# Kernel tuning notes

Measured on AMD Instinct MI355X. Metric: run time of the kernel, lower is better.

Reference implementation:

```python
import jax, jax.numpy as jnp
import numpy as np

B, N, D, H = 2, 256, 512, 8
DK = D // H


def _lin(x, w, b):
    # torch nn.Linear: y = x @ W.T + b, W is [out, in]
    return jnp.matmul(x, w.T) + b


def setup_inputs() -> dict:
    key = jax.random.key(0)
    ks = jax.random.split(key, 12)
    std = 0.02
    inp = {
        "x": jax.random.normal(ks[0], (B, N, D), jnp.float32),
        "batched_graphs": jax.random.normal(ks[1], (B, N, N, D), jnp.float32) * std,
        "mask": jnp.zeros((B, N, N), dtype=bool),
    }
    names = ["wq", "wk", "wv", "wo", "wl", "wr", "wrk", "wrv"]
    for i, n in enumerate(names):
        inp[n] = jax.random.normal(ks[2 + i], (D, D), jnp.float32) * std
        inp["b" + n[1:]] = jnp.zeros((D,), jnp.float32)
    return inp


def reference(x, batched_graphs, mask,
              wq, bq, wk, bk, wv, bv, wo, bo,
              wl, bl, wr, br, wrk, brk, wrv, brv):
    # update_relations: per-edge key/value maps
    graphs_k = _lin(batched_graphs, wrk, brk).reshape(B, N, N, H, DK)
    graphs_v = _lin(batched_graphs, wrv, brv).reshape(B, N, N, H, DK)

    query = _lin(x, wq, bq).reshape(B, N, H, DK)
    key_ = _lin(x, wk, bk).reshape(B, N, H, DK)
    value = _lin(x, wv, bv).reshape(B, N, H, DK)

    scores_k = jnp.einsum("bxhd,byhd->bxyh", query, key_)
    scores_g = jnp.einsum("bxhd,bxyhd->bxyh", query, graphs_k)
    scores = (scores_k + scores_g) / np.sqrt(DK).astype(np.float32)
    scores = jnp.where(mask[..., None], jnp.float32(-1e9), scores)
    p_attn = jax.nn.softmax(scores, axis=2)  # over key nodes y

    x_v = jnp.einsum("bxyh,byhd->bxhd", p_attn, value)
    x_g = jnp.einsum("bxyh,bxyhd->bxhd", p_attn, graphs_v)
    out = (x_v + x_g).reshape(B, N, D)

    # relation update: outer sum of left/right projections
    x_left = _lin(out, wl, bl)[:, :, None, :]   # [B,N,1,D]
    x_right = _lin(out, wr, br)[:, None, :, :]  # [B,1,N,D]
    new_graphs = x_left + x_right               # [B,N,N,D]

    return _lin(out, wo, bo), new_graphs
```

## Files before the change

### kernel.cpp

```cpp
#include <hip/hip_runtime.h>

#define BB 2
#define NN 256
#define DD 512
#define HH 8

#define SCL 0.18033688f

typedef float f4raw __attribute__((ext_vector_type(4)));

__device__ __forceinline__ float dot4(float4 a, float4 b) {
    return a.x*b.x + a.y*b.y + a.z*b.z + a.w*b.w;
}

__device__ __forceinline__ float4 f4fma(float s, float4 a, float4 acc) {
    acc.x += s * a.x; acc.y += s * a.y; acc.z += s * a.z; acc.w += s * a.w;
    return acc;
}

__device__ __forceinline__ float4 f4mul(float s, float4 a) {
    a.x *= s; a.y *= s; a.z *= s; a.w *= s; return a;
}

__device__ __forceinline__ float4 f4add(float4 a, float4 b) {
    a.x += b.x; a.y += b.y; a.z += b.z; a.w += b.w; return a;
}

__device__ __forceinline__ void gload_lds16(const void* g, void* l) {
    __builtin_amdgcn_global_load_lds(
        (const __attribute__((address_space(1))) unsigned int*)g,
        (__attribute__((address_space(3))) unsigned int*)l, 16, 0, 0);
}

__device__ __forceinline__ void stage_swz(const char* rowbase, float4* dst, int w, int lane) {
    #pragma unroll
    for (int j = 0; j < 4; ++j) {
        const int f0 = w * 256 + j * 64;
        const int y = f0 >> 7;
        const int c = (f0 & 127) + lane;
        gload_lds16(rowbase + (size_t)y * 2048 + ((size_t)(c ^ y) << 4), &dst[f0]);
    }
}

__device__ __forceinline__ void stageG(const char* Grow, int tt, int w, int lane, float4* dst) {
    #pragma unroll
    for (int r = 0; r < 2; ++r) {
        const int yr = 2 * w + r;
        const char* src = Grow + (size_t)(tt * 8 + yr) * 2048;
        #pragma unroll
        for (int j = 0; j < 2; ++j) {
            const int c = j * 64 + lane;
            gload_lds16(src + ((size_t)(c ^ yr) << 4), &dst[r * 128 + j * 64]);
        }
    }
}

__global__ __launch_bounds__(64) void kProj(
    const float* __restrict__ in_,
    const float* __restrict__ w0, const float* __restrict__ b0,
    const float* __restrict__ w1, const float* __restrict__ b1,
    const float* __restrict__ w2, const float* __restrict__ b2,
    float* __restrict__ o0, float* __restrict__ o1, float* __restrict__ o2)
{
    __shared__ float4 xs[2][32 * 5];
    __shared__ float4 ws[2][32 * 5];

    const int t = threadIdx.x;
    const int blk = blockIdx.x;
    const int proj = blk >> 8;
    const int rem = blk & 255;
    const int row0 = (rem >> 4) * 32;
    const int col0 = (rem & 15) * 32;

    const float* W; const float* Bp; float* O;
    if (proj == 0)      { W = w0; Bp = b0; O = o0; }
    else if (proj == 1) { W = w1; Bp = b1; O = o1; }
    else                { W = w2; Bp = b2; O = o2; }

    const float4* X4 = (const float4*)in_ + (size_t)row0 * 128;
    const float4* W4 = (const float4*)W  + (size_t)col0 * 128;

    const int sr = t >> 2, se = t & 3;
    const int ty = t >> 3, tx = t & 7;

    float4 rx0 = X4[(size_t)sr * 128 + se];
    float4 rx1 = X4[(size_t)(sr + 16) * 128 + se];
    float4 rw0 = W4[(size_t)sr * 128 + se];
    float4 rw1 = W4[(size_t)(sr + 16) * 128 + se];
    xs[0][sr * 5 + se] = rx0;  xs[0][(sr + 16) * 5 + se] = rx1;
    ws[0][sr * 5 + se] = rw0;  ws[0][(sr + 16) * 5 + se] = rw1;

    float acc[4][4] = {};

    for (int q = 0; q < 32; ++q) {
        __syncthreads();
        const int cur = q & 1;
        if (q < 31) {
            const int ko = (q + 1) * 4;
            rx0 = X4[(size_t)sr * 128 + ko + se];
            rx1 = X4[(size_t)(sr + 16) * 128 + ko + se];
            rw0 = W4[(size_t)sr * 128 + ko + se];
            rw1 = W4[(size_t)(sr + 16) * 128 + ko + se];
        }
        const float4* xb = xs[cur];
        const float4* wb = ws[cur];
        #pragma unroll
        for (int e4 = 0; e4 < 4; ++e4) {
            float4 xr[4], wc[4];
            #pragma unroll
            for (int i = 0; i < 4; ++i) xr[i] = xb[(ty + 8 * i) * 5 + e4];
            #pragma unroll
            for (int j = 0; j < 4; ++j) wc[j] = wb[(tx + 8 * j) * 5 + e4];
            #pragma unroll
            for (int i = 0; i < 4; ++i)
                #pragma unroll
                for (int j = 0; j < 4; ++j)
                    acc[i][j] += dot4(xr[i], wc[j]);
        }
        if (q < 31) {
            const int nxt = cur ^ 1;
            xs[nxt][sr * 5 + se] = rx0;  xs[nxt][(sr + 16) * 5 + se] = rx1;
            ws[nxt][sr * 5 + se] = rw0;  ws[nxt][(sr + 16) * 5 + se] = rw1;
        }
    }

    float bb[4];
    #pragma unroll
    for (int j = 0; j < 4; ++j) bb[j] = Bp[col0 + tx + 8 * j];
    #pragma unroll
    for (int i = 0; i < 4; ++i) {
        const int orow = row0 + ty + 8 * i;
        #pragma unroll
        for (int j = 0; j < 4; ++j)
            O[(size_t)orow * DD + col0 + tx + 8 * j] = acc[i][j] + bb[j];
    }
}

__global__ __launch_bounds__(256) void kQkp(
    const float* __restrict__ q, const float* __restrict__ wrk,
    float* __restrict__ qkp)
{
    __shared__ float qs[8 * 64];
    const int t = threadIdx.x;
    const int blk = blockIdx.x;
    const int rowg = blk >> 5;
    const int h = (blk >> 2) & 7;
    const int eq = blk & 3;
    const int row0 = rowg * 8;
    {
        const int r = t >> 5, d2 = (t & 31) * 2;
        const float2 tmp = *(const float2*)(q + (size_t)(row0 + r) * DD + h * 64 + d2);
        qs[r * 64 + d2] = tmp.x; qs[r * 64 + d2 + 1] = tmp.y;
    }
    __syncthreads();
    const int e = eq * 128 + (t & 127);
    const int rp = (t >> 7) * 4;
    const float* wcol = wrk + (size_t)(h * 64) * DD + e;
    float a0 = 0, a1 = 0, a2 = 0, a3 = 0;
    #pragma unroll 8
    for (int d = 0; d < 64; ++d) {
        const float wv = wcol[(size_t)d * DD];
        a0 += qs[(rp + 0) * 64 + d] * wv;
        a1 += qs[(rp + 1) * 64 + d] * wv;
        a2 += qs[(rp + 2) * 64 + d] * wv;
        a3 += qs[(rp + 3) * 64 + d] * wv;
    }
    qkp[((size_t)(row0 + rp + 0) * HH + h) * DD + e] = a0;
    qkp[((size_t)(row0 + rp + 1) * HH + h) * DD + e] = a1;
    qkp[((size_t)(row0 + rp + 2) * HH + h) * DD + e] = a2;
    qkp[((size_t)(row0 + rp + 3) * HH + h) * DD + e] = a3;
}

__global__ __launch_bounds__(256) void kSk(
    const float* __restrict__ q, const float* __restrict__ k,
    const unsigned char* __restrict__ mask, float* __restrict__ sk)
{
    __shared__ float qs[8 * 65];
    __shared__ float ks[64 * 65];
    const int t = threadIdx.x;
    const int blk = blockIdx.x;
    const int b  = blk >> 10;
    const int h  = (blk >> 7) & 7;
    const int xt = (blk >> 2) & 31;
    const int yt = blk & 3;
    const int x0 = xt * 8, y0 = yt * 64;
    {
        const int r = t >> 5, d2 = (t & 31) * 2;
        const float2 tmp = *(const float2*)(q + (size_t)(b * NN + x0 + r) * DD + h * 64 + d2);
        qs[r * 65 + d2] = tmp.x; qs[r * 65 + d2 + 1] = tmp.y;
    }
    #pragma unroll
    for (int j = 0; j < 8; ++j) {
        const int f = t + 256 * j;
        const int r = f >> 5, d2 = (f & 31) * 2;
        const float2 tmp = *(const float2*)(k + (size_t)(b * NN + y0 + r) * DD + h * 64 + d2);
        ks[r * 65 + d2] = tmp.x; ks[r * 65 + d2 + 1] = tmp.y;
    }
    __syncthreads();
    const int xi = t >> 5, yg = t & 31;
    float a0 = 0, a1 = 0;
    #pragma unroll 8
    for (int d = 0; d < 64; ++d) {
        const float qv = qs[xi * 65 + d];
        a0 += qv * ks[(yg * 2 + 0) * 65 + d];
        a1 += qv * ks[(yg * 2 + 1) * 65 + d];
    }
    a0 *= SCL; a1 *= SCL;
    const unsigned char* mrow = mask + (size_t)(b * NN + x0 + xi) * NN;
    const int gy = y0 + yg * 2;
    if (mrow[gy + 0]) a0 = -1e9f;
    if (mrow[gy + 1]) a1 = -1e9f;
    float2 st; st.x = a0; st.y = a1;
    *(float2*)(sk + ((size_t)(b * NN + x0 + xi) * HH + h) * NN + gy) = st;
}

__global__ __launch_bounds__(256, 2) void kC(
    const float* __restrict__ G, const float* __restrict__ sk,
    const float* __restrict__ qkp, const float* __restrict__ v,
    float* __restrict__ pg, float* __restrict__ pxv,
    float* __restrict__ pm, float* __restrict__ pl)
{
    __shared__ float4 Gdb[2][4][256];
    __shared__ float4 qk4[1024];
    __shared__ float  sk_lds[512];
    __shared__ float  s_st[512];

    const int t = threadIdx.x;
    const int lane = t & 63;
    const int w = t >> 6;
    const int blk = blockIdx.x;
    const int part = blk & 3;
    const int bid = blk >> 2;
    const int b = bid >> 8;
    const int ybase = part * 64;

    const int s_ = lane & 15;
    const int g  = lane >> 4;
    const int h0_ = 2 * g, h1_ = h0_ + 1;
    const int yr0 = 2 * w, yr1 = yr0 + 1;

    const char* Grow = (const char*)(G + (size_t)bid * NN * DD) + (size_t)ybase * 2048;
    const float* skb = sk + (size_t)bid * HH * NN;
    const float4* vb4 = (const float4*)(v + (size_t)(b * NN) * DD);

    const int f0p = 2 * t, f1p = 2 * t + 1;
    const float skv0 = skb[(f0p & 7) * NN + ybase + (f0p >> 3)];
    const float skv1 = skb[(f1p & 7) * NN + ybase + (f1p >> 3)];
    stage_swz((const char*)(qkp + (size_t)bid * HH * DD), qk4, w, lane);
    float4 va0 = vb4[(size_t)(ybase + yr0) * 128 + 32 * g + s_];
    float4 vb0 = vb4[(size_t)(ybase + yr0) * 128 + 32 * g + 16 + s_];
    float4 va1 = vb4[(size_t)(ybase + yr1) * 128 + 32 * g + s_];
    float4 vb1 = vb4[(size_t)(ybase + yr1) * 128 + 32 * g + 16 + s_];
    stageG(Grow, 0, w, lane, &Gdb[0][w][0]);
    asm volatile("s_waitcnt vmcnt(4)" ::: "memory");
    __builtin_amdgcn_sched_barrier(0);
    sk_lds[f0p] = skv0;
    sk_lds[f1p] = skv1;
    __syncthreads();

    float4 gA[8], gB[8];
    float m[8], l[8];
    #pragma unroll
    for (int h = 0; h < 8; ++h) {
        gA[h] = make_float4(0, 0, 0, 0);
        gB[h] = make_float4(0, 0, 0, 0);
        m[h] = -3e38f; l[h] = 0.f;
    }
    float4 xva = {0, 0, 0, 0}, xvb = {0, 0, 0, 0};
    float4 nva0 = va0, nvb0 = vb0, nva1 = va1, nvb1 = vb1;

    int cb = 0;
    #pragma unroll 1
    for (int tt = 0; tt < 8; ++tt) {
        const int ry0 = tt * 8 + yr0, ry1 = ry0 + 1;

        __builtin_amdgcn_sched_barrier(0);
        if (tt < 7) {
            stageG(Grow, tt + 1, w, lane, &Gdb[cb ^ 1][w][0]);
            const int ngy0 = ybase + (tt + 1) * 8 + yr0;
            nva0 = vb4[(size_t)ngy0 * 128 + 32 * g + s_];
            nvb0 = vb4[(size_t)ngy0 * 128 + 32 * g + 16 + s_];
            nva1 = vb4[(size_t)(ngy0 + 1) * 128 + 32 * g + s_];
            nvb1 = vb4[(size_t)(ngy0 + 1) * 128 + 32 * g + 16 + s_];
            asm volatile("s_waitcnt vmcnt(8)" ::: "memory");
        } else {
            asm volatile("s_waitcnt vmcnt(0)" ::: "memory");
        }
        __builtin_amdgcn_sched_barrier(0);

        const float4* gb = &Gdb[cb][w][0];

        {
            float a00 = 0, a01 = 0, a10 = 0, a11 = 0;
            #pragma unroll
            for (int i = 0; i < 8; ++i) {
                const int e4 = i * 16 + s_;
                const float4 g0 = gb[(e4 ^ yr0)];
                const float4 g1 = gb[128 + (e4 ^ yr1)];
                const float4 p0 = qk4[h0_ * 128 + (e4 ^ h0_)];
                const float4 p1 = qk4[h1_ * 128 + (e4 ^ h1_)];
                a00 += dot4(g0, p0); a01 += dot4(g0, p1);
                a10 += dot4(g1, p0); a11 += dot4(g1, p1);
            }
            #pragma unroll
            for (int mm = 1; mm < 16; mm <<= 1) {
                a00 += __shfl_xor(a00, mm); a01 += __shfl_xor(a01, mm);
                a10 += __shfl_xor(a10, mm); a11 += __shfl_xor(a11, mm);
            }
            if (s_ < 4) {
                const int yy = s_ & 1, hh = s_ >> 1;
                const float val = yy ? (hh ? a11 : a10) : (hh ? a01 : a00);
                const int h = h0_ + hh;
                const int ry = yy ? ry1 : ry0;
                s_st[ry * 8 + h] = val * SCL + sk_lds[ry * 8 + h];
            }
        }

        const float4 sva = *(const float4*)&s_st[ry0 * 8];
        const float4 svb = *(const float4*)&s_st[ry0 * 8 + 4];
        const float4 svc = *(const float4*)&s_st[ry1 * 8];
        const float4 svd = *(const float4*)&s_st[ry1 * 8 + 4];
        const float s0[8] = {sva.x, sva.y, sva.z, sva.w, svb.x, svb.y, svb.z, svb.w};
        const float s1[8] = {svc.x, svc.y, svc.z, svc.w, svd.x, svd.y, svd.z, svd.w};

        const float4 gr0a = gb[(lane ^ yr0)];
        const float4 gr0b = gb[((lane + 64) ^ yr0)];
        const float4 gr1a = gb[128 + (lane ^ yr1)];
        const float4 gr1b = gb[128 + ((lane + 64) ^ yr1)];

        float p0a = 0, p1a = 0, rsa = 1, p0b = 0, p1b = 0, rsb = 1;
        #pragma unroll
        for (int h = 0; h < 8; ++h) {
            const float mn = fmaxf(m[h], fmaxf(s0[h], s1[h]));
            const float rs = exp2f(m[h] - mn);
            const float p0 = exp2f(s0[h] - mn);
            const float p1 = exp2f(s1[h] - mn);
            m[h] = mn;
            l[h] = l[h] * rs + p0 + p1;
            gA[h] = f4fma(p1, gr1a, f4fma(p0, gr0a, f4mul(rs, gA[h])));
            gB[h] = f4fma(p1, gr1b, f4fma(p0, gr0b, f4mul(rs, gB[h])));
            if (h == h0_) { p0a = p0; p1a = p1; rsa = rs; }
            if (h == h1_) { p0b = p0; p1b = p1; rsb = rs; }
        }
        xva = f4fma(p1a, va1, f4fma(p0a, va0, f4mul(rsa, xva)));
        xvb = f4fma(p1b, vb1, f4fma(p0b, vb0, f4mul(rsb, xvb)));
        va0 = nva0; vb0 = nvb0; va1 = nva1; vb1 = nvb1;
        cb ^= 1;
    }

    asm volatile("s_waitcnt vmcnt(0)" ::: "memory");
    __syncthreads();
    float* ml = sk_lds;
    if (lane == 0) {
        #pragma unroll
        for (int h = 0; h < 8; ++h) { ml[w * 16 + h] = m[h]; ml[w * 16 + 8 + h] = l[h]; }
    }
    __syncthreads();

    float ea = 1.f, eb = 1.f;
    float Mv[8], Lv[8];
    #pragma unroll
    for (int h = 0; h < 8; ++h) {
        const float q0 = ml[h], q1 = ml[16 + h], q2 = ml[32 + h], q3 = ml[48 + h];
        const float Mh = fmaxf(fmaxf(q0, q1), fmaxf(q2, q3));
        const float Lh = exp2f(q0 - Mh) * ml[8 + h]  + exp2f(q1 - Mh) * ml[24 + h]
                       + exp2f(q2 - Mh) * ml[40 + h] + exp2f(q3 - Mh) * ml[56 + h];
        Mv[h] = Mh; Lv[h] = Lh;
        const float e = exp2f(m[h] - Mh);
        gA[h] = f4mul(e, gA[h]);
        gB[h] = f4mul(e, gB[h]);
        if (h == h0_) ea = e;
        if (h == h1_) eb = e;
    }
    xva = f4mul(ea, xva);
    xvb = f4mul(eb, xvb);

    float4* rA = &Gdb[0][0][0];
    float4* rB = &Gdb[1][0][0];
    float4* xs_ = qk4;
    xs_[w * 128 + 32 * g + s_] = xva;
    xs_[w * 128 + 32 * g + 16 + s_] = xvb;
    if (w == 2) {
        #pragma unroll
        for (int h = 0; h < 8; ++h) { rA[h * 128 + lane] = gA[h]; rA[h * 128 + 64 + lane] = gB[h]; }
    }
    if (w == 3) {
        #pragma unroll
        for (int h = 0; h < 8; ++h) { rB[h * 128 + lane] = gA[h]; rB[h * 128 + 64 + lane] = gB[h]; }
    }
    __syncthreads();
    if (w == 0) {
        #pragma unroll
        for (int h = 0; h < 8; ++h) {
            gA[h] = f4add(gA[h], rA[h * 128 + lane]);
            gB[h] = f4add(gB[h], rA[h * 128 + 64 + lane]);
        }
    }
    if (w == 1) {
        #pragma unroll
        for (int h = 0; h < 8; ++h) {
            gA[h] = f4add(gA[h], rB[h * 128 + lane]);
            gB[h] = f4add(gB[h], rB[h * 128 + 64 + lane]);
        }
    }
    __syncthreads();
    if (w == 1) {
        #pragma unroll
        for (int h = 0; h < 8; ++h) { rA[h * 128 + lane] = gA[h]; rA[h * 128 + 64 + lane] = gB[h]; }
    }
    __syncthreads();
    if (w == 0) {
        float4* pgb = (float4*)pg + (size_t)blk * 1024;
        #pragma unroll
        for (int h = 0; h < 8; ++h) {
            gA[h] = f4add(gA[h], rA[h * 128 + lane]);
            gB[h] = f4add(gB[h], rA[h * 128 + 64 + lane]);
            pgb[h * 128 + lane] = gA[h];
            pgb[h * 128 + 64 + lane] = gB[h];
        }
        float4 xa = f4add(f4add(xs_[32 * g + s_],            xs_[128 + 32 * g + s_]),
                          f4add(xs_[256 + 32 * g + s_],      xs_[384 + 32 * g + s_]));
        float4 xb = f4add(f4add(xs_[32 * g + 16 + s_],       xs_[128 + 32 * g + 16 + s_]),
                          f4add(xs_[256 + 32 * g + 16 + s_], xs_[384 + 32 * g + 16 + s_]));
        float4* pxb = (float4*)pxv + (size_t)blk * 128;
        pxb[32 * g + s_] = xa;
        pxb[32 * g + 16 + s_] = xb;
        if (lane == 0) {
            #pragma unroll
            for (int h = 0; h < 8; ++h) { pm[blk * 8 + h] = Mv[h]; pl[blk * 8 + h] = Lv[h]; }
        }
    }
}

__global__ __launch_bounds__(256) void kM(
    const float* __restrict__ pg, const float* __restrict__ pxv,
    const float* __restrict__ pm, const float* __restrict__ pl,
    const float* __restrict__ wrv, const float* __restrict__ brv,
    float* __restrict__ om)
{
    __shared__ float4 gc[512];
    __shared__ float xvs[256];
    __shared__ float wexp[16], Ls[4];
    const int t = threadIdx.x;
    const int blk = blockIdx.x;
    const int bid = blk >> 1;
    const int half = blk & 1;
    const int h0 = half * 4;
    __shared__ float mlds[16], llds[16];
    if (t < 16) {
        const int i = t >> 2, hh = t & 3;
        mlds[t] = pm[bid * 32 + i * 8 + h0 + hh];
        llds[t] = pl[bid * 32 + i * 8 + h0 + hh];
    }
    __syncthreads();
    if (t < 4) {
        float M = mlds[t];
        #pragma unroll
        for (int i = 1; i < 4; ++i) M = fmaxf(M, mlds[i * 4 + t]);
        float L = 0;
        #pragma unroll
        for (int i = 0; i < 4; ++i) {
            const float wv = exp2f(mlds[i * 4 + t] - M);
            wexp[i * 4 + t] = wv;
            L += wv * llds[i * 4 + t];
        }
        Ls[t] = L;
    }
    __syncthreads();
    const int c4 = t & 127;
    #pragma unroll
    for (int r = 0; r < 2; ++r) {
        const int hh = (t >> 7) * 2 + r;
        float4 acc = {0, 0, 0, 0};
        #pragma unroll
        for (int i = 0; i < 4; ++i) {
            const float wv = wexp[i * 4 + hh];
            const float4 g = ((const float4*)pg)[((size_t)bid * 4 + i) * 1024 + (size_t)(h0 + hh) * 128 + c4];
            acc.x += wv * g.x; acc.y += wv * g.y; acc.z += wv * g.z; acc.w += wv * g.w;
        }
        gc[hh * 128 + c4] = acc;
    }
    {
        const int hh = t >> 6;
        float s = 0;
        #pragma unroll
        for (int i = 0; i < 4; ++i)
            s += wexp[i * 4 + hh] * pxv[((size_t)bid * 4 + i) * DD + half * 256 + t];
        xvs[t] = s;
    }
    __syncthreads();
    const int o = half * 256 + t;
    const int hl = t >> 6;
    const float4* wr4 = (const float4*)(wrv + (size_t)o * DD);
    float acc = 0;
    #pragma unroll 4
    for (int e4 = 0; e4 < 128; ++e4) acc += dot4(wr4[e4], gc[hl * 128 + e4]);
    om[(size_t)bid * DD + o] = (xvs[t] + acc) / Ls[hl] + brv[o];
}

__global__ __launch_bounds__(256) void kE(
    const float* __restrict__ xl, const float* __restrict__ xr,
    float* __restrict__ ng)
{
    const int t = threadIdx.x;
    const int blk = blockIdx.x;
    const int bid = blk >> 2;
    const int yc = blk & 3;
    const int b = bid >> 8;
    const int o4 = t & 127;
    const int yh = t >> 7;
    const float4 left = ((const float4*)xl)[(size_t)bid * 128 + o4];
    const float4* xr4 = (const float4*)xr + (size_t)b * NN * 128;
    f4raw* out4 = (f4raw*)ng + (size_t)bid * NN * 128;
    for (int y = yc * 64 + yh; y < yc * 64 + 64; y += 2) {
        const float4 rr = xr4[y * 128 + o4];
        f4raw s;
        s.x = left.x + rr.x; s.y = left.y + rr.y;
        s.z = left.z + rr.z; s.w = left.w + rr.w;
        __builtin_nontemporal_store(s, &out4[y * 128 + o4]);
    }
}

extern "C" void kernel_launch(void* const* d_in, const int* in_sizes, int n_in,
                              void* d_out, int out_size, void* d_ws, size_t ws_size,
                              hipStream_t stream)
{
    (void)in_sizes; (void)n_in; (void)out_size; (void)ws_size;
    const float* x    = (const float*)d_in[0];
    const float* G    = (const float*)d_in[1];
    const unsigned char* mask = (const unsigned char*)d_in[2];
    const float* wq  = (const float*)d_in[3];  const float* bq  = (const float*)d_in[4];
    const float* wk  = (const float*)d_in[5];  const float* bk  = (const float*)d_in[6];
    const float* wv  = (const float*)d_in[7];  const float* bv  = (const float*)d_in[8];
    const float* wo  = (const float*)d_in[9];  const float* bo  = (const float*)d_in[10];
    const float* wl  = (const float*)d_in[11]; const float* bl  = (const float*)d_in[12];
    const float* wr  = (const float*)d_in[13]; const float* br  = (const float*)d_in[14];
    const float* wrk = (const float*)d_in[15];
    const float* wrv = (const float*)d_in[17]; const float* brv = (const float*)d_in[18];

    float* out  = (float*)d_out;
    float* fout = out;
    float* ng   = out + (size_t)BB * NN * DD;

    const size_t ng_f  = (size_t)BB * NN * NN * DD;
    const size_t row_f = (size_t)BB * NN * DD;
    const size_t total = row_f * 52 + 32768;
    float* base = ng + ng_f - total;
    float* q    = base;
    float* k    = q   + row_f;
    float* vv_  = k   + row_f;
    float* qkp  = vv_ + row_f;
    float* skp  = qkp + row_f * 8;
    float* pg   = skp + row_f * 4;
    float* pxv  = pg  + row_f * 32;
    float* pm   = pxv + row_f * 4;
    float* pl   = pm  + 16384;
    float* om   = pl  + 16384;
    float* xl = (float*)d_ws;
    float* xr = xl + row_f;

    kProj<<<768, 64, 0, stream>>>(x, wq, bq, wk, bk, wv, bv, q, k, vv_);
    kQkp <<<2048, 256, 0, stream>>>(q, wrk, qkp);
    kSk  <<<2048, 256, 0, stream>>>(q, k, mask, skp);
    kC   <<<2048, 256, 0, stream>>>(G, skp, qkp, vv_, pg, pxv, pm, pl);
    kM   <<<1024, 256, 0, stream>>>(pg, pxv, pm, pl, wrv, brv, om);
    kProj<<<768, 64, 0, stream>>>(om, wo, bo, wl, bl, wr, br, fout, xl, xr);
    kE   <<<2048, 256, 0, stream>>>(xl, xr, ng);
}
```

Baseline: 311.1 us.

## Merge qkp and score kernels; process one graph row per wave per step in kC

Folds the kQkp and kSk launches into one kernel, kQS, that picks its role from the block index, removing one launch and letting both workloads run side by side. In kC, each wave now handles one G row per iteration over 16 steps instead of two rows over 8. This halves the G double buffer in LDS and cuts register pressure, since V is loaded inside the loop rather than prefetched. The cross-wave reduction becomes a serial loop over three stages. The trade-off is more loop iterations and barriers, and V loads that are no longer prefetched and may stall each step.

```diff
diff --git a/kernel.cpp b/kernel.cpp
--- a/kernel.cpp
+++ b/kernel.cpp
@@ -42,16 +42,12 @@
     }
 }
 
-__device__ __forceinline__ void stageG(const char* Grow, int tt, int w, int lane, float4* dst) {
-    #pragma unroll
-    for (int r = 0; r < 2; ++r) {
-        const int yr = 2 * w + r;
-        const char* src = Grow + (size_t)(tt * 8 + yr) * 2048;
-        #pragma unroll
-        for (int j = 0; j < 2; ++j) {
-            const int c = j * 64 + lane;
-            gload_lds16(src + ((size_t)(c ^ yr) << 4), &dst[r * 128 + j * 64]);
-        }
+__device__ __forceinline__ void stageG1(const char* Grow, int tt, int w, int lane, float4* dst) {
+    const char* src = Grow + (size_t)(tt * 4 + w) * 2048;
+    #pragma unroll
+    for (int j = 0; j < 2; ++j) {
+        const int c = j * 64 + lane;
+        gload_lds16(src + ((size_t)(c ^ w) << 4), &dst[j * 64]);
     }
 }
 
@@ -136,82 +132,81 @@
     }
 }
 
-__global__ __launch_bounds__(256) void kQkp(
+__global__ __launch_bounds__(256) void kQS(
     const float* __restrict__ q, const float* __restrict__ wrk,
-    float* __restrict__ qkp)
+    const float* __restrict__ k, const unsigned char* __restrict__ mask,
+    float* __restrict__ qkp, float* __restrict__ sk)
 {
-    __shared__ float qs[8 * 64];
+    __shared__ float sm[4680];
     const int t = threadIdx.x;
-    const int blk = blockIdx.x;
-    const int rowg = blk >> 5;
-    const int h = (blk >> 2) & 7;
-    const int eq = blk & 3;
-    const int row0 = rowg * 8;
-    {
-        const int r = t >> 5, d2 = (t & 31) * 2;
-        const float2 tmp = *(const float2*)(q + (size_t)(row0 + r) * DD + h * 64 + d2);
-        qs[r * 64 + d2] = tmp.x; qs[r * 64 + d2 + 1] = tmp.y;
-    }
-    __syncthreads();
-    const int e = eq * 128 + (t & 127);
-    const int rp = (t >> 7) * 4;
-    const float* wcol = wrk + (size_t)(h * 64) * DD + e;
-    float a0 = 0, a1 = 0, a2 = 0, a3 = 0;
-    #pragma unroll 8
-    for (int d = 0; d < 64; ++d) {
-        const float wv = wcol[(size_t)d * DD];
-        a0 += qs[(rp + 0) * 64 + d] * wv;
-        a1 += qs[(rp + 1) * 64 + d] * wv;
-        a2 += qs[(rp + 2) * 64 + d] * wv;
-        a3 += qs[(rp + 3) * 64 + d] * wv;
-    }
-    qkp[((size_t)(row0 + rp + 0) * HH + h) * DD + e] = a0;
-    qkp[((size_t)(row0 + rp + 1) * HH + h) * DD + e] = a1;
-    qkp[((size_t)(row0 + rp + 2) * HH + h) * DD + e] = a2;
-    qkp[((size_t)(row0 + rp + 3) * HH + h) * DD + e] = a3;
-}
-
-__global__ __launch_bounds__(256) void kSk(
-    const float* __restrict__ q, const float* __restrict__ k,
-    const unsigned char* __restrict__ mask, float* __restrict__ sk)
-{
-    __shared__ float qs[8 * 65];
-    __shared__ float ks[64 * 65];
-    const int t = threadIdx.x;
-    const int blk = blockIdx.x;
-    const int b  = blk >> 10;
-    const int h  = (blk >> 7) & 7;
-    const int xt = (blk >> 2) & 31;
-    const int yt = blk & 3;
-    const int x0 = xt * 8, y0 = yt * 64;
-    {
-        const int r = t >> 5, d2 = (t & 31) * 2;
-        const float2 tmp = *(const float2*)(q + (size_t)(b * NN + x0 + r) * DD + h * 64 + d2);
-        qs[r * 65 + d2] = tmp.x; qs[r * 65 + d2 + 1] = tmp.y;
-    }
-    #pragma unroll
-    for (int j = 0; j < 8; ++j) {
-        const int f = t + 256 * j;
-        const int r = f >> 5, d2 = (f & 31) * 2;
-        const float2 tmp = *(const float2*)(k + (size_t)(b * NN + y0 + r) * DD + h * 64 + d2);
-        ks[r * 65 + d2] = tmp.x; ks[r * 65 + d2 + 1] = tmp.y;
-    }
-    __syncthreads();
-    const int xi = t >> 5, yg = t & 31;
-    float a0 = 0, a1 = 0;
-    #pragma unroll 8
-    for (int d = 0; d < 64; ++d) {
-        const float qv = qs[xi * 65 + d];
-        a0 += qv * ks[(yg * 2 + 0) * 65 + d];
-        a1 += qv * ks[(yg * 2 + 1) * 65 + d];
-    }
-    a0 *= SCL; a1 *= SCL;
-    const unsigned char* mrow = mask + (size_t)(b * NN + x0 + xi) * NN;
-    const int gy = y0 + yg * 2;
-    if (mrow[gy + 0]) a0 = -1e9f;
-    if (mrow[gy + 1]) a1 = -1e9f;
-    float2 st; st.x = a0; st.y = a1;
-    *(float2*)(sk + ((size_t)(b * NN + x0 + xi) * HH + h) * NN + gy) = st;
+    const int blk0 = blockIdx.x;
+
+    if (blk0 < 2048) {
+        float* qs = sm;
+        const int rowg = blk0 >> 5;
+        const int h = (blk0 >> 2) & 7;
+        const int eq = blk0 & 3;
+        const int row0 = rowg * 8;
+        {
+            const int r = t >> 5, d2 = (t & 31) * 2;
+            const float2 tmp = *(const float2*)(q + (size_t)(row0 + r) * DD + h * 64 + d2);
+            qs[r * 64 + d2] = tmp.x; qs[r * 64 + d2 + 1] = tmp.y;
+        }
+        __syncthreads();
+        const int e = eq * 128 + (t & 127);
+        const int rp = (t >> 7) * 4;
+        const float* wcol = wrk + (size_t)(h * 64) * DD + e;
+        float a0 = 0, a1 = 0, a2 = 0, a3 = 0;
+        #pragma unroll 8
+        for (int d = 0; d < 64; ++d) {
+            const float wv = wcol[(size_t)d * DD];
+            a0 += qs[(rp + 0) * 64 + d] * wv;
+            a1 += qs[(rp + 1) * 64 + d] * wv;
+            a2 += qs[(rp + 2) * 64 + d] * wv;
+            a3 += qs[(rp + 3) * 64 + d] * wv;
+        }
+        qkp[((size_t)(row0 + rp + 0) * HH + h) * DD + e] = a0;
+        qkp[((size_t)(row0 + rp + 1) * HH + h) * DD + e] = a1;
+        qkp[((size_t)(row0 + rp + 2) * HH + h) * DD + e] = a2;
+        qkp[((size_t)(row0 + rp + 3) * HH + h) * DD + e] = a3;
+    } else {
+        const int blk = blk0 - 2048;
+        float* qs = sm;
+        float* ks = sm + 8 * 65;
+        const int b  = blk >> 10;
+        const int h  = (blk >> 7) & 7;
+        const int xt = (blk >> 2) & 31;
+        const int yt = blk & 3;
+        const int x0 = xt * 8, y0 = yt * 64;
+        {
+            const int r = t >> 5, d2 = (t & 31) * 2;
+            const float2 tmp = *(const float2*)(q + (size_t)(b * NN + x0 + r) * DD + h * 64 + d2);
+            qs[r * 65 + d2] = tmp.x; qs[r * 65 + d2 + 1] = tmp.y;
+        }
+        #pragma unroll
+        for (int j = 0; j < 8; ++j) {
+            const int f = t + 256 * j;
+            const int r = f >> 5, d2 = (f & 31) * 2;
+            const float2 tmp = *(const float2*)(k + (size_t)(b * NN + y0 + r) * DD + h * 64 + d2);
+            ks[r * 65 + d2] = tmp.x; ks[r * 65 + d2 + 1] = tmp.y;
+        }
+        __syncthreads();
+        const int xi = t >> 5, yg = t & 31;
+        float a0 = 0, a1 = 0;
+        #pragma unroll 8
+        for (int d = 0; d < 64; ++d) {
+            const float qv = qs[xi * 65 + d];
+            a0 += qv * ks[(yg * 2 + 0) * 65 + d];
+            a1 += qv * ks[(yg * 2 + 1) * 65 + d];
+        }
+        a0 *= SCL; a1 *= SCL;
+        const unsigned char* mrow = mask + (size_t)(b * NN + x0 + xi) * NN;
+        const int gy = y0 + yg * 2;
+        if (mrow[gy + 0]) a0 = -1e9f;
+        if (mrow[gy + 1]) a1 = -1e9f;
+        float2 st; st.x = a0; st.y = a1;
+        *(float2*)(sk + ((size_t)(b * NN + x0 + xi) * HH + h) * NN + gy) = st;
+    }
 }
 
 __global__ __launch_bounds__(256, 2) void kC(
@@ -220,7 +215,7 @@
     float* __restrict__ pg, float* __restrict__ pxv,
     float* __restrict__ pm, float* __restrict__ pl)
 {
-    __shared__ float4 Gdb[2][4][256];
+    __shared__ float4 Gdb[2][4][128];
     __shared__ float4 qk4[1024];
     __shared__ float  sk_lds[512];
     __shared__ float  s_st[512];
@@ -237,7 +232,6 @@
     const int s_ = lane & 15;
     const int g  = lane >> 4;
     const int h0_ = 2 * g, h1_ = h0_ + 1;
-    const int yr0 = 2 * w, yr1 = yr0 + 1;
 
     const char* Grow = (const char*)(G + (size_t)bid * NN * DD) + (size_t)ybase * 2048;
     const float* skb = sk + (size_t)bid * HH * NN;
@@ -247,12 +241,8 @@
     const float skv0 = skb[(f0p & 7) * NN + ybase + (f0p >> 3)];
     const float skv1 = skb[(f1p & 7) * NN + ybase + (f1p >> 3)];
     stage_swz((const char*)(qkp + (size_t)bid * HH * DD), qk4, w, lane);
-    float4 va0 = vb4[(size_t)(ybase + yr0) * 128 + 32 * g + s_];
-    float4 vb0 = vb4[(size_t)(ybase + yr0) * 128 + 32 * g + 16 + s_];
-    float4 va1 = vb4[(size_t)(ybase + yr1) * 128 + 32 * g + s_];
-    float4 vb1 = vb4[(size_t)(ybase + yr1) * 128 + 32 * g + 16 + s_];
-    stageG(Grow, 0, w, lane, &Gdb[0][w][0]);
-    asm volatile("s_waitcnt vmcnt(4)" ::: "memory");
+    stageG1(Grow, 0, w, lane, &Gdb[0][w][0]);
+    asm volatile("s_waitcnt vmcnt(2)" ::: "memory");
     __builtin_amdgcn_sched_barrier(0);
     sk_lds[f0p] = skv0;
     sk_lds[f1p] = skv1;
@@ -267,22 +257,20 @@
         m[h] = -3e38f; l[h] = 0.f;
     }
     float4 xva = {0, 0, 0, 0}, xvb = {0, 0, 0, 0};
-    float4 nva0 = va0, nvb0 = vb0, nva1 = va1, nvb1 = vb1;
 
     int cb = 0;
     #pragma unroll 1
-    for (int tt = 0; tt < 8; ++tt) {
-        const int ry0 = tt * 8 + yr0, ry1 = ry0 + 1;
-
+    for (int tt = 0; tt < 16; ++tt) {
+        const int gy = ybase + tt * 4 + w;
+        const int ry = tt * 4 + w;
+
+        const float4 va0 = vb4[(size_t)gy * 128 + 32 * g + s_];
+        const float4 vb0 = vb4[(size_t)gy * 128 + 32 * g + 16 + s_];
         __builtin_amdgcn_sched_barrier(0);
-        if (tt < 7) {
-            stageG(Grow, tt + 1, w, lane, &Gdb[cb ^ 1][w][0]);
-            const int ngy0 = ybase + (tt + 1) * 8 + yr0;
-            nva0 = vb4[(size_t)ngy0 * 128 + 32 * g + s_];
-            nvb0 = vb4[(size_t)ngy0 * 128 + 32 * g + 16 + s_];
-            nva1 = vb4[(size_t)(ngy0 + 1) * 128 + 32 * g + s_];
-            nvb1 = vb4[(size_t)(ngy0 + 1) * 128 + 32 * g + 16 + s_];
-            asm volatile("s_waitcnt vmcnt(8)" ::: "memory");
+        if (tt < 15)
+            stageG1(Grow, tt + 1, w, lane, &Gdb[cb ^ 1][w][0]);
+        if (tt < 15) {
+            asm volatile("s_waitcnt vmcnt(2)" ::: "memory");
         } else {
             asm volatile("s_waitcnt vmcnt(0)" ::: "memory");
         }
@@ -291,60 +279,47 @@
         const float4* gb = &Gdb[cb][w][0];
 
         {
-            float a00 = 0, a01 = 0, a10 = 0, a11 = 0;
+            float a00 = 0, a01 = 0;
             #pragma unroll
             for (int i = 0; i < 8; ++i) {
                 const int e4 = i * 16 + s_;
-                const float4 g0 = gb[(e4 ^ yr0)];
-                const float4 g1 = gb[128 + (e4 ^ yr1)];
-                const float4 p0 = qk4[h0_ * 128 + (e4 ^ h0_)];
-                const float4 p1 = qk4[h1_ * 128 + (e4 ^ h1_)];
-                a00 += dot4(g0, p0); a01 += dot4(g0, p1);
-                a10 += dot4(g1, p0); a11 += dot4(g1, p1);
+                const float4 g0 = gb[(e4 ^ w)];
+                a00 += dot4(g0, qk4[h0_ * 128 + (e4 ^ h0_)]);
+                a01 += dot4(g0, qk4[h1_ * 128 + (e4 ^ h1_)]);
             }
             #pragma unroll
             for (int mm = 1; mm < 16; mm <<= 1) {
                 a00 += __shfl_xor(a00, mm); a01 += __shfl_xor(a01, mm);
-                a10 += __shfl_xor(a10, mm); a11 += __shfl_xor(a11, mm);
             }
-            if (s_ < 4) {
-                const int yy = s_ & 1, hh = s_ >> 1;
-                const float val = yy ? (hh ? a11 : a10) : (hh ? a01 : a00);
-                const int h = h0_ + hh;
-                const int ry = yy ? ry1 : ry0;
+            if (s_ < 2) {
+                const float val = (s_ == 0) ? a00 : a01;
+                const int h = h0_ + s_;
                 s_st[ry * 8 + h] = val * SCL + sk_lds[ry * 8 + h];
             }
         }
 
-        const float4 sva = *(const float4*)&s_st[ry0 * 8];
-        const float4 svb = *(const float4*)&s_st[ry0 * 8 + 4];
-        const float4 svc = *(const float4*)&s_st[ry1 * 8];
-        const float4 svd = *(const float4*)&s_st[ry1 * 8 + 4];
+        const float4 sva = *(const float4*)&s_st[ry * 8];
+        const float4 svb = *(const float4*)&s_st[ry * 8 + 4];
         const float s0[8] = {sva.x, sva.y, sva.z, sva.w, svb.x, svb.y, svb.z, svb.w};
-        const float s1[8] = {svc.x, svc.y, svc.z, svc.w, svd.x, svd.y, svd.z, svd.w};
-
-        const float4 gr0a = gb[(lane ^ yr0)];
-        const float4 gr0b = gb[((lane + 64) ^ yr0)];
-        const float4 gr1a = gb[128 + (lane ^ yr1)];
-        const float4 gr1b = gb[128 + ((lane + 64) ^ yr1)];
-
-        float p0a = 0, p1a = 0, rsa = 1, p0b = 0, p1b = 0, rsb = 1;
+
+        const float4 gr0a = gb[(lane ^ w)];
+        const float4 gr0b = gb[((lane + 64) ^ w)];
+
+        float p0a = 0, rsa = 1, p0b = 0, rsb = 1;
         #pragma unroll
         for (int h = 0; h < 8; ++h) {
-            const float mn = fmaxf(m[h], fmaxf(s0[h], s1[h]));
+            const float mn = fmaxf(m[h], s0[h]);
             const float rs = exp2f(m[h] - mn);
             const float p0 = exp2f(s0[h] - mn);
-            const float p1 = exp2f(s1[h] - mn);
             m[h] = mn;
-            l[h] = l[h] * rs + p0 + p1;
-            gA[h] = f4fma(p1, gr1a, f4fma(p0, gr0a, f4mul(rs, gA[h])));
-            gB[h] = f4fma(p1, gr1b, f4fma(p0, gr0b, f4mul(rs, gB[h])));
-            if (h == h0_) { p0a = p0; p1a = p1; rsa = rs; }
-            if (h == h1_) { p0b = p0; p1b = p1; rsb = rs; }
-        }
-        xva = f4fma(p1a, va1, f4fma(p0a, va0, f4mul(rsa, xva)));
-        xvb = f4fma(p1b, vb1, f4fma(p0b, vb0, f4mul(rsb, xvb)));
-        va0 = nva0; vb0 = nvb0; va1 = nva1; vb1 = nvb1;
+            l[h] = l[h] * rs + p0;
+            gA[h] = f4fma(p0, gr0a, f4mul(rs, gA[h]));
+            gB[h] = f4fma(p0, gr0b, f4mul(rs, gB[h]));
+            if (h == h0_) { p0a = p0; rsa = rs; }
+            if (h == h1_) { p0b = p0; rsb = rs; }
+        }
+        xva = f4fma(p0a, va0, f4mul(rsa, xva));
+        xvb = f4fma(p0b, vb0, f4mul(rsb, xvb));
         cb ^= 1;
     }
 
@@ -376,45 +351,31 @@
     xvb = f4mul(eb, xvb);
 
     float4* rA = &Gdb[0][0][0];
-    float4* rB = &Gdb[1][0][0];
     float4* xs_ = qk4;
     xs_[w * 128 + 32 * g + s_] = xva;
     xs_[w * 128 + 32 * g + 16 + s_] = xvb;
-    if (w == 2) {
-        #pragma unroll
-        for (int h = 0; h < 8; ++h) { rA[h * 128 + lane] = gA[h]; rA[h * 128 + 64 + lane] = gB[h]; }
-    }
-    if (w == 3) {
-        #pragma unroll
-        for (int h = 0; h < 8; ++h) { rB[h * 128 + lane] = gA[h]; rB[h * 128 + 64 + lane] = gB[h]; }
-    }
-    __syncthreads();
-    if (w == 0) {
-        #pragma unroll
-        for (int h = 0; h < 8; ++h) {
-            gA[h] = f4add(gA[h], rA[h * 128 + lane]);
-            gB[h] = f4add(gB[h], rA[h * 128 + 64 + lane]);
-        }
-    }
-    if (w == 1) {
-        #pragma unroll
-        for (int h = 0; h < 8; ++h) {
-            gA[h] = f4add(gA[h], rB[h * 128 + lane]);
-            gB[h] = f4add(gB[h], rB[h * 128 + 64 + lane]);
-        }
-    }
-    __syncthreads();
-    if (w == 1) {
-        #pragma unroll
-        for (int h = 0; h < 8; ++h) { rA[h * 128 + lane] = gA[h]; rA[h * 128 + 64 + lane] = gB[h]; }
-    }
-    __syncthreads();
+
+    #pragma unroll 1
+    for (int r = 3; r >= 1; --r) {
+        __syncthreads();
+        if (w == r) {
+            #pragma unroll
+            for (int h = 0; h < 8; ++h) { rA[h * 128 + lane] = gA[h]; rA[h * 128 + 64 + lane] = gB[h]; }
+        }
+        __syncthreads();
+        if (w == r - 1) {
+            #pragma unroll
+            for (int h = 0; h < 8; ++h) {
+                gA[h] = f4add(gA[h], rA[h * 128 + lane]);
+                gB[h] = f4add(gB[h], rA[h * 128 + 64 + lane]);
+            }
+        }
+    }
+
     if (w == 0) {
         float4* pgb = (float4*)pg + (size_t)blk * 1024;
         #pragma unroll
         for (int h = 0; h < 8; ++h) {
-            gA[h] = f4add(gA[h], rA[h * 128 + lane]);
-            gB[h] = f4add(gB[h], rA[h * 128 + 64 + lane]);
             pgb[h * 128 + lane] = gA[h];
             pgb[h * 128 + 64 + lane] = gB[h];
         }
@@ -560,8 +521,7 @@
     float* xr = xl + row_f;
 
     kProj<<<768, 64, 0, stream>>>(x, wq, bq, wk, bk, wv, bv, q, k, vv_);
-    kQkp <<<2048, 256, 0, stream>>>(q, wrk, qkp);
-    kSk  <<<2048, 256, 0, stream>>>(q, k, mask, skp);
+    kQS  <<<4096, 256, 0, stream>>>(q, wrk, k, mask, qkp, skp);
     kC   <<<2048, 256, 0, stream>>>(G, skp, qkp, vv_, pg, pxv, pm, pl);
     kM   <<<1024, 256, 0, stream>>>(pg, pxv, pm, pl, wrv, brv, om);
     kProj<<<768, 64, 0, stream>>>(om, wo, bo, wl, bl, wr, br, fout, xl, xr);
```

Result: no change. 308.5 us (-0.8%).
